# Performance work log

Hardware: AMD Instinct MI355X
Metric: run time of the kernel (lower is better)

The kernel has to match this reference:

```python
import jax, jax.numpy as jnp
import numpy as np

N_HEAD = 16


def setup_inputs() -> dict:
    key = jax.random.key(0)
    k1, k2, k3 = jax.random.split(key, 3)
    B, T, C = 4, 1024, 1024
    x = jax.random.normal(k1, (B, T, C), dtype=jnp.float32)
    w_attn = jax.random.normal(k2, (3 * C, C), dtype=jnp.float32) * 0.02
    w_proj = jax.random.normal(k3, (C, C), dtype=jnp.float32) * 0.02
    return {"x": x, "w_attn": w_attn, "w_proj": w_proj}


def reference(x, w_attn, w_proj):
    B, T, C = x.shape
    H = N_HEAD
    hs = C // H
    scale = 1.0 / np.sqrt(hs).astype(np.float32)

    qkv = x @ w_attn.T                         # [B, T, 3C]
    q, k, v = jnp.split(qkv, 3, axis=-1)
    q = q.reshape(B, T, H, hs).transpose(0, 2, 1, 3)   # [B, H, T, hs]
    k = k.reshape(B, T, H, hs).transpose(0, 2, 1, 3)
    v = v.reshape(B, T, H, hs).transpose(0, 2, 1, 3)

    scores = jnp.einsum('bhqd,bhkd->bhqk', q, k) * scale   # [B, H, T, T]
    causal = jnp.tril(jnp.ones((T, T), dtype=bool))
    scores = jnp.where(causal, scores, -jnp.inf)

    att = jax.nn.sigmoid(scores)                # sigmoid attention, not softmax
    # Bernoulli straight-through sampling (value = sample, grad flows via att)
    samp_key = jax.random.fold_in(jax.random.key(0), 42)
    samples = jax.random.bernoulli(samp_key, att).astype(att.dtype)
    att = att + jax.lax.stop_gradient(samples - att)

    y = jnp.einsum('bhqk,bhkd->bhqd', att, v)   # [B, H, T, hs]
    att_sum = att.sum(axis=-1)                  # [B, H, T]
    att_var = (att * (1.0 - att)).sum(axis=-1)  # [B, H, T]

    y = y.transpose(0, 2, 1, 3).reshape(B, T, C)
    y = y @ w_proj.T
    return (y, att_sum, att_var)
```

## Files before the change

kernel.cpp:

```cpp
#include <hip/hip_runtime.h>
#include <stdint.h>


#define T_SEQ 1024
#define QKV_LD 3072

typedef __attribute__((ext_vector_type(8))) short bf16x8;
typedef __attribute__((ext_vector_type(4))) float f32x4;
typedef __attribute__((ext_vector_type(4))) unsigned int u32x4;

typedef __attribute__((address_space(3))) uint32_t lds_u32;
typedef __attribute__((address_space(1))) const uint32_t g_u32;

#define ROTL(x, d) __builtin_amdgcn_alignbit((x), (x), 32 - (d))

__device__ __forceinline__ void threefry2x32(uint32_t k0, uint32_t k1,
                                             uint32_t x0, uint32_t x1,
                                             uint32_t &o0, uint32_t &o1) {
  uint32_t ks2 = k0 ^ k1 ^ 0x1BD11BDAu;
#define TF_R4(a, b, c, d)                                                      \
  x0 += x1; x1 = ROTL(x1, a); x1 ^= x0;                                        \
  x0 += x1; x1 = ROTL(x1, b); x1 ^= x0;                                        \
  x0 += x1; x1 = ROTL(x1, c); x1 ^= x0;                                        \
  x0 += x1; x1 = ROTL(x1, d); x1 ^= x0;
  x0 += k0; x1 += k1;
  TF_R4(13, 15, 26, 6)
  x0 += k1; x1 += ks2 + 1u;
  TF_R4(17, 29, 16, 24)
  x0 += ks2; x1 += k0 + 2u;
  TF_R4(13, 15, 26, 6)
  x0 += k0; x1 += k1 + 3u;
  TF_R4(17, 29, 16, 24)
  x0 += k1; x1 += ks2 + 4u;
  TF_R4(13, 15, 26, 6)
  x0 += ks2; x1 += k0 + 5u;
  o0 = x0; o1 = x1;
#undef TF_R4
}

__device__ __forceinline__ unsigned short f2bf(float f) {
  uint32_t u = __float_as_uint(f);
  u += 0x7FFFu + ((u >> 16) & 1u);
  return (unsigned short)(u >> 16);
}

#define N_X4  1048576
#define N_WA4 786432
#define N_WP4 262144

__global__ __launch_bounds__(256) void cvt3_bf16(const float4* __restrict__ x,
                                                 const float4* __restrict__ wa,
                                                 const float4* __restrict__ wp,
                                                 uint2* __restrict__ out) {
  size_t i = (size_t)blockIdx.x * 256 + threadIdx.x;
  const float4* src;
  size_t off;
  if (i < N_X4) { src = x; off = i; }
  else if (i < N_X4 + N_WA4) { src = wa; off = i - N_X4; }
  else { src = wp; off = i - (N_X4 + N_WA4); }
  float4 v = src[off];
  uint2 o;
  o.x = (uint32_t)f2bf(v.x) | ((uint32_t)f2bf(v.y) << 16);
  o.y = (uint32_t)f2bf(v.z) | ((uint32_t)f2bf(v.w) << 16);
  out[i] = o;
}

template <int OUT_BF16>
__global__ __launch_bounds__(256) void gemm_bf16(const unsigned short* __restrict__ A,
                                                 const unsigned short* __restrict__ B,
                                                 void* __restrict__ Cout,
                                                 int M, int N, int K) {
  __shared__ unsigned short As[128 * 32];
  __shared__ unsigned short Bs[128 * 32];

  const int t = threadIdx.x;
  const int lane = t & 63, w = t >> 6;
  const int g = lane >> 4, lr = lane & 15;
  const int rw = w >> 1, cw = w & 1;
  const int bm = blockIdx.x * 128, bn = blockIdx.y * 128;

  const unsigned short* Ag = A + (size_t)(bm + 32 * w + (lane >> 2)) * K + 8 * (lane & 3);
  const unsigned short* Bg = B + (size_t)(bn + 32 * w + (lane >> 2)) * K + 8 * (lane & 3);
  lds_u32* Al0 = (lds_u32*)&As[(32 * w) * 32];
  lds_u32* Al1 = (lds_u32*)&As[(32 * w + 16) * 32];
  lds_u32* Bl0 = (lds_u32*)&Bs[(32 * w) * 32];
  lds_u32* Bl1 = (lds_u32*)&Bs[(32 * w + 16) * 32];

  f32x4 acc[4][4];
#pragma unroll
  for (int i = 0; i < 4; ++i)
#pragma unroll
    for (int j = 0; j < 4; ++j) acc[i][j] = (f32x4){0.f, 0.f, 0.f, 0.f};

  for (int k0 = 0; k0 < K; k0 += 32) {
    __syncthreads();
    __builtin_amdgcn_global_load_lds((g_u32*)(const void*)(Ag + k0), Al0, 16, 0, 0);
    __builtin_amdgcn_global_load_lds((g_u32*)(const void*)(Ag + k0 + (size_t)16 * K), Al1, 16, 0, 0);
    __builtin_amdgcn_global_load_lds((g_u32*)(const void*)(Bg + k0), Bl0, 16, 0, 0);
    __builtin_amdgcn_global_load_lds((g_u32*)(const void*)(Bg + k0 + (size_t)16 * K), Bl1, 16, 0, 0);
    __syncthreads();

    bf16x8 af[4], bfr[4];
#pragma unroll
    for (int i = 0; i < 4; ++i)
      af[i] = *(const bf16x8*)&As[(64 * rw + 16 * i + lr) * 32 + 8 * g];
#pragma unroll
    for (int j = 0; j < 4; ++j)
      bfr[j] = *(const bf16x8*)&Bs[(64 * cw + 16 * j + lr) * 32 + 8 * g];
#pragma unroll
    for (int i = 0; i < 4; ++i)
#pragma unroll
      for (int j = 0; j < 4; ++j)
        acc[i][j] = __builtin_amdgcn_mfma_f32_16x16x32_bf16(af[i], bfr[j], acc[i][j], 0, 0, 0);
  }

#pragma unroll
  for (int i = 0; i < 4; ++i)
#pragma unroll
    for (int j = 0; j < 4; ++j)
#pragma unroll
      for (int r = 0; r < 4; ++r) {
        const size_t row = bm + 64 * rw + 16 * i + 4 * g + r;
        const size_t col = bn + 64 * cw + 16 * j + lr;
        if (OUT_BF16)
          ((unsigned short*)Cout)[row * N + col] = f2bf(acc[i][j][r]);
        else
          ((float*)Cout)[row * N + col] = acc[i][j][r];
      }
}

__constant__ uint8_t QT_OF[136] = {
    0, 1, 1, 2, 2, 2, 3, 3, 3, 3, 4, 4, 4, 4, 4, 5, 5, 5, 5, 5, 5,
    6, 6, 6, 6, 6, 6, 6, 7, 7, 7, 7, 7, 7, 7, 7,
    8, 8, 8, 8, 8, 8, 8, 8, 8, 9, 9, 9, 9, 9, 9, 9, 9, 9, 9,
    10, 10, 10, 10, 10, 10, 10, 10, 10, 10, 10,
    11, 11, 11, 11, 11, 11, 11, 11, 11, 11, 11, 11,
    12, 12, 12, 12, 12, 12, 12, 12, 12, 12, 12, 12, 12,
    13, 13, 13, 13, 13, 13, 13, 13, 13, 13, 13, 13, 13, 13,
    14, 14, 14, 14, 14, 14, 14, 14, 14, 14, 14, 14, 14, 14, 14,
    15, 15, 15, 15, 15, 15, 15, 15, 15, 15, 15, 15, 15, 15, 15, 15};

#define TFI_STEP(a)                                                            \
  _Pragma("unroll")                                                            \
  for (int j = 0; j < 4; ++j) {                                                \
    X0[j] += X1[j]; X1[j] = ROTL(X1[j], a); X1[j] ^= X0[j];                    \
  }
#define TFI_R4(a, b, c, d) TFI_STEP(a) TFI_STEP(b) TFI_STEP(c) TFI_STEP(d)
#define TFI_INJ(i0, i1)                                                        \
  _Pragma("unroll")                                                            \
  for (int j = 0; j < 4; ++j) { X0[j] += (i0); X1[j] += (i1); }

__global__ __launch_bounds__(256, 8) void attn_sample(const unsigned short* __restrict__ qkv,
                                                      unsigned short* __restrict__ Pbits) {
  __shared__ uint32_t Ks4[64 * 32];

  const int t = threadIdx.x;
  const int lane = t & 63, w = t >> 6;
  const int g = lane >> 4, lr = lane & 15;
  const int bid = blockIdx.x;
  const int bh = 8 * (bid & 7) + ((bid >> 3) & 7);
  const int id = bid >> 6;
  const int qt = QT_OF[id];
  const int kt = id - ((qt * (qt + 1)) >> 1);
  const int b = bh >> 4, h = bh & 15;
  const int q0 = qt * 64 + 16 * w;
  const int kt64 = kt * 64;
  const bool diag = (kt == qt);

  uint32_t dk0, dk1;
  threefry2x32(0u, 0u, 0u, 42u, dk0, dk1);
  const uint32_t ks2 = dk0 ^ dk1 ^ 0x1BD11BDAu;

  const unsigned short* kb = qkv + (size_t)(b * T_SEQ + kt64) * QKV_LD + 1024 + h * 64;
  {
    const int r = t >> 2, s4 = t & 3;
    const unsigned short* src = kb + (size_t)r * QKV_LD + 8 * s4;
    u32x4 v0 = *(const u32x4*)(src);
    u32x4 v1 = *(const u32x4*)(src + 32);
    const int sw = (r & 7) << 2;
    *(u32x4*)&Ks4[r * 32 + ((4 * s4) ^ sw)] = v0;
    *(u32x4*)&Ks4[r * 32 + ((4 * s4 + 16) ^ sw)] = v1;
  }
  const unsigned short* qr = qkv + (size_t)(b * T_SEQ + q0 + lr) * QKV_LD + h * 64 + 8 * g;
  const bf16x8 aq0 = *(const bf16x8*)qr;
  const bf16x8 aq1 = *(const bf16x8*)(qr + 32);
  __syncthreads();

  const int swzr = (lr & 7) << 2;
  unsigned short* prow = Pbits + ((size_t)((bh << 10) + q0)) * 64 + kt * 4;

#pragma unroll
  for (int c = 0; c < 4; ++c) {
    bool pred[4] = {false, false, false, false};
    if (!diag || c <= w) {
      const uint32_t* krow = &Ks4[(16 * c + lr) * 32];
      bf16x8 bk0 = *(const bf16x8*)&krow[(4 * g) ^ swzr];
      bf16x8 bk1 = *(const bf16x8*)&krow[(4 * g + 16) ^ swzr];
      f32x4 sa = __builtin_amdgcn_mfma_f32_16x16x32_bf16(aq0, bk0, (f32x4){0.f, 0.f, 0.f, 0.f}, 0, 0, 0);
      sa = __builtin_amdgcn_mfma_f32_16x16x32_bf16(aq1, bk1, sa, 0, 0, 0);

      const int kg = kt64 + 16 * c + lr;
      const uint32_t idxc =
          ((uint32_t)bh << 20) | ((uint32_t)(q0 + 4 * g) << 10) | (uint32_t)kg;

      float e[4];
#pragma unroll
      for (int r = 0; r < 4; ++r)
        e[r] = __builtin_exp2f(sa[r] * -0.18033688011112042f);

      uint32_t X0[4], X1[4];
#pragma unroll
      for (int r = 0; r < 4; ++r) { X0[r] = dk0; X1[r] = idxc + ((uint32_t)r << 10) + dk1; }
      TFI_R4(13, 15, 26, 6)
      TFI_INJ(dk1, ks2 + 1u)
      TFI_R4(17, 29, 16, 24)
      TFI_INJ(ks2, dk0 + 2u)
      TFI_R4(13, 15, 26, 6)
      TFI_INJ(dk0, dk1 + 3u)
      TFI_R4(17, 29, 16, 24)
      TFI_INJ(dk1, ks2 + 4u)
      TFI_R4(13, 15, 26, 6)
      TFI_INJ(ks2, dk0 + 5u)

#pragma unroll
      for (int r = 0; r < 4; ++r) {
        const int qg = q0 + 4 * g + r;
        float u = __uint_as_float(0x3F800000u | ((X0[r] ^ X1[r]) >> 9)) - 1.0f;
        pred[r] = (fmaf(u, e[r], u) < 1.0f) & (kg <= qg);
      }
    }
#pragma unroll
    for (int r = 0; r < 4; ++r) {
      unsigned long long m = __ballot(pred[r]);
      if (lr == 0)
        prow[(size_t)(4 * g + r) * 64 + c] = (unsigned short)((m >> (16 * g)) & 0xFFFFu);
    }
  }
}

__global__ __launch_bounds__(256) void attn_pv(const unsigned short* __restrict__ qkv,
                                               const unsigned short* __restrict__ Pbits,
                                               unsigned short* __restrict__ yatt,
                                               float* __restrict__ att_sum,
                                               float* __restrict__ att_var) {
  __shared__ uint32_t Vt4[64 * 32];

  const int t = threadIdx.x;
  const int lane = t & 63, w = t >> 6;
  const int g = lane >> 4, lr = lane & 15;
  const int bid = blockIdx.x;
  const int bh = 8 * (bid & 7) + ((bid >> 3) & 7);
  const int qt = 15 - (bid >> 6);
  const int b = bh >> 4, h = bh & 15;
  const int q0 = qt * 64 + 16 * w;

  const int swzr = (lr & 7) << 2;
  const unsigned short* prow = Pbits + ((size_t)((bh << 10) + q0 + lr)) * 64;

  f32x4 yacc[4];
#pragma unroll
  for (int c = 0; c < 4; ++c) yacc[c] = (f32x4){0.f, 0.f, 0.f, 0.f};
  uint32_t rs = 0;

#pragma unroll 1
  for (int kt = 0; kt <= qt; ++kt) {
    __syncthreads();
    {
      const int k2 = 2 * (t & 31), d0 = 8 * (t >> 5);
      const unsigned short* vsrc =
          qkv + (size_t)(b * T_SEQ + kt * 64 + k2) * QKV_LD + 2048 + h * 64 + d0;
      union { u32x4 v; unsigned short us[8]; } va, vb2;
      va.v = *(const u32x4*)(vsrc);
      vb2.v = *(const u32x4*)(vsrc + QKV_LD);
#pragma unroll
      for (int jj = 0; jj < 8; ++jj) {
        uint32_t pw = (uint32_t)va.us[jj] | ((uint32_t)vb2.us[jj] << 16);
        Vt4[(d0 + jj) * 32 + ((t & 31) ^ ((jj & 7) << 2))] = pw;
      }
    }
    __syncthreads();

    const uint64_t bits = *(const uint64_t*)(prow + kt * 4);
    rs += (uint32_t)__popcll(bits);

#pragma unroll
    for (int ks = 0; ks < 2; ++ks) {
      const uint32_t byte = (uint32_t)(bits >> (32 * ks + 8 * g)) & 0xFFu;
      union { uint32_t u[4]; bf16x8 v; } pa;
#pragma unroll
      for (int j = 0; j < 4; ++j) {
        pa.u[j] = ((byte >> (2 * j)) & 1u ? 0x3F80u : 0u) |
                  ((byte >> (2 * j + 1)) & 1u ? 0x3F800000u : 0u);
      }
#pragma unroll
      for (int c = 0; c < 4; ++c) {
        bf16x8 vb = *(const bf16x8*)&Vt4[(16 * c + lr) * 32 + ((4 * g + 16 * ks) ^ swzr)];
        yacc[c] = __builtin_amdgcn_mfma_f32_16x16x32_bf16(pa.v, vb, yacc[c], 0, 0, 0);
      }
    }
  }

  const size_t yb = (size_t)(b * T_SEQ + q0) * 1024 + h * 64;
#pragma unroll
  for (int c = 0; c < 4; ++c)
#pragma unroll
    for (int r = 0; r < 4; ++r)
      yatt[yb + (size_t)(4 * g + r) * 1024 + 16 * c + lr] = f2bf(yacc[c][r]);

  if (g == 0) att_sum[(size_t)bh * T_SEQ + q0 + lr] = (float)rs;
  if (lane < 16) att_var[(size_t)bh * T_SEQ + q0 + lane] = 0.f;
}

extern "C" void kernel_launch(void* const* d_in, const int* in_sizes, int n_in,
                              void* d_out, int out_size, void* d_ws, size_t ws_size,
                              hipStream_t stream) {
  (void)in_sizes; (void)n_in; (void)out_size; (void)ws_size;
  const float* x      = (const float*)d_in[0];
  const float* w_attn = (const float*)d_in[1];
  const float* w_proj = (const float*)d_in[2];

  float* y_out      = (float*)d_out;
  float* attsum_out = y_out + (size_t)4 * 1024 * 1024;
  float* attvar_out = attsum_out + (size_t)4 * 16 * 1024;

  unsigned short* ws_us = (unsigned short*)d_ws;
  unsigned short* x_bf    = ws_us;
  unsigned short* wa_bf   = x_bf + (size_t)4 * 1024 * 1024;
  unsigned short* wp_bf   = wa_bf + (size_t)3 * 1024 * 1024;
  unsigned short* qkv_bf  = wp_bf + (size_t)1024 * 1024;
  unsigned short* yatt_bf = qkv_bf + (size_t)4096 * 3072;
  unsigned short* pbits   = yatt_bf + (size_t)4096 * 1024;

  dim3 blk(256);
  cvt3_bf16<<<dim3(8192), blk, 0, stream>>>((const float4*)x, (const float4*)w_attn,
                                            (const float4*)w_proj, (uint2*)x_bf);
  gemm_bf16<1><<<dim3(32, 24), blk, 0, stream>>>(x_bf, wa_bf, (void*)qkv_bf, 4096, 3072, 1024);
  attn_sample<<<dim3(8704), blk, 0, stream>>>(qkv_bf, pbits);
  attn_pv<<<dim3(1024), blk, 0, stream>>>(qkv_bf, pbits, yatt_bf, attsum_out, attvar_out);
  gemm_bf16<0><<<dim3(32, 8), blk, 0, stream>>>(yatt_bf, wp_bf, (void*)y_out, 4096, 1024, 1024);
}
```

Measured before the change: 173.1 us.

## Pair causal query tiles per block in PV and simplify diagonal masking in sampling

The PV kernel now runs 512 blocks, and each block handles two query tiles (qt = 15-p and qt = p), so every block does the same total number of key tiles. This balances the triangular causal workload across blocks. In the sampling kernel, the causal mask for diagonal tiles is applied as a precomputed bitmask on the ballot result instead of a per-lane comparison, and the branch uses a wave-uniform index. Skipped chunks write zero directly. The risk is that halving the grid lowers occupancy and adds a serial second pass per block.

```diff
diff --git a/kernel.cpp b/kernel.cpp
--- a/kernel.cpp
+++ b/kernel.cpp
@@ -140,16 +140,6 @@
     14, 14, 14, 14, 14, 14, 14, 14, 14, 14, 14, 14, 14, 14, 14,
     15, 15, 15, 15, 15, 15, 15, 15, 15, 15, 15, 15, 15, 15, 15, 15};
 
-#define TFI_STEP(a)                                                            \
-  _Pragma("unroll")                                                            \
-  for (int j = 0; j < 4; ++j) {                                                \
-    X0[j] += X1[j]; X1[j] = ROTL(X1[j], a); X1[j] ^= X0[j];                    \
-  }
-#define TFI_R4(a, b, c, d) TFI_STEP(a) TFI_STEP(b) TFI_STEP(c) TFI_STEP(d)
-#define TFI_INJ(i0, i1)                                                        \
-  _Pragma("unroll")                                                            \
-  for (int j = 0; j < 4; ++j) { X0[j] += (i0); X1[j] += (i1); }
-
 __global__ __launch_bounds__(256, 8) void attn_sample(const unsigned short* __restrict__ qkv,
                                                       unsigned short* __restrict__ Pbits) {
   __shared__ uint32_t Ks4[64 * 32];
@@ -166,6 +156,7 @@
   const int q0 = qt * 64 + 16 * w;
   const int kt64 = kt * 64;
   const bool diag = (kt == qt);
+  const int ws = __builtin_amdgcn_readfirstlane(w);
 
   uint32_t dk0, dk1;
   threefry2x32(0u, 0u, 0u, 42u, dk0, dk1);
@@ -189,10 +180,19 @@
   const int swzr = (lr & 7) << 2;
   unsigned short* prow = Pbits + ((size_t)((bh << 10) + q0)) * 64 + kt * 4;
 
+#define TFI_STEP(a)                                                            \
+  _Pragma("unroll")                                                            \
+  for (int j = 0; j < 4; ++j) {                                                \
+    X0[j] += X1[j]; X1[j] = ROTL(X1[j], a); X1[j] ^= X0[j];                    \
+  }
+#define TFI_R4(a, b, c, d) TFI_STEP(a) TFI_STEP(b) TFI_STEP(c) TFI_STEP(d)
+#define TFI_INJ(i0, i1)                                                        \
+  _Pragma("unroll")                                                            \
+  for (int j = 0; j < 4; ++j) { X0[j] += (i0); X1[j] += (i1); }
+
 #pragma unroll
   for (int c = 0; c < 4; ++c) {
-    bool pred[4] = {false, false, false, false};
-    if (!diag || c <= w) {
+    if (!diag || c <= ws) {
       const uint32_t* krow = &Ks4[(16 * c + lr) * 32];
       bf16x8 bk0 = *(const bf16x8*)&krow[(4 * g) ^ swzr];
       bf16x8 bk1 = *(const bf16x8*)&krow[(4 * g + 16) ^ swzr];
@@ -224,18 +224,31 @@
 
 #pragma unroll
       for (int r = 0; r < 4; ++r) {
-        const int qg = q0 + 4 * g + r;
         float u = __uint_as_float(0x3F800000u | ((X0[r] ^ X1[r]) >> 9)) - 1.0f;
-        pred[r] = (fmaf(u, e[r], u) < 1.0f) & (kg <= qg);
+        unsigned long long m = __ballot(fmaf(u, e[r], u) < 1.0f);
+        if (diag) {
+          const int d = 16 * (ws - c) + r;
+          unsigned long long cm = 0ull;
+#pragma unroll
+          for (int gg = 0; gg < 4; ++gg) {
+            const int thr = d + 4 * gg;
+            const uint32_t pc = (thr >= 15) ? 0xFFFFu : ((2u << thr) - 1u);
+            cm |= (unsigned long long)pc << (16 * gg);
+          }
+          m &= cm;
+        }
+        if (lr == 0)
+          prow[(size_t)(4 * g + r) * 64 + c] = (unsigned short)(m >> (16 * g));
       }
+    } else {
+#pragma unroll
+      for (int r = 0; r < 4; ++r)
+        if (lr == 0) prow[(size_t)(4 * g + r) * 64 + c] = 0;
     }
-#pragma unroll
-    for (int r = 0; r < 4; ++r) {
-      unsigned long long m = __ballot(pred[r]);
-      if (lr == 0)
-        prow[(size_t)(4 * g + r) * 64 + c] = (unsigned short)((m >> (16 * g)) & 0xFFFFu);
-    }
-  }
+  }
+#undef TFI_STEP
+#undef TFI_R4
+#undef TFI_INJ
 }
 
 __global__ __launch_bounds__(256) void attn_pv(const unsigned short* __restrict__ qkv,
@@ -250,65 +263,69 @@
   const int g = lane >> 4, lr = lane & 15;
   const int bid = blockIdx.x;
   const int bh = 8 * (bid & 7) + ((bid >> 3) & 7);
-  const int qt = 15 - (bid >> 6);
+  const int p = bid >> 6;
   const int b = bh >> 4, h = bh & 15;
-  const int q0 = qt * 64 + 16 * w;
-
   const int swzr = (lr & 7) << 2;
-  const unsigned short* prow = Pbits + ((size_t)((bh << 10) + q0 + lr)) * 64;
-
-  f32x4 yacc[4];
-#pragma unroll
-  for (int c = 0; c < 4; ++c) yacc[c] = (f32x4){0.f, 0.f, 0.f, 0.f};
-  uint32_t rs = 0;
 
 #pragma unroll 1
-  for (int kt = 0; kt <= qt; ++kt) {
-    __syncthreads();
-    {
-      const int k2 = 2 * (t & 31), d0 = 8 * (t >> 5);
-      const unsigned short* vsrc =
-          qkv + (size_t)(b * T_SEQ + kt * 64 + k2) * QKV_LD + 2048 + h * 64 + d0;
-      union { u32x4 v; unsigned short us[8]; } va, vb2;
-      va.v = *(const u32x4*)(vsrc);
-      vb2.v = *(const u32x4*)(vsrc + QKV_LD);
-#pragma unroll
-      for (int jj = 0; jj < 8; ++jj) {
-        uint32_t pw = (uint32_t)va.us[jj] | ((uint32_t)vb2.us[jj] << 16);
-        Vt4[(d0 + jj) * 32 + ((t & 31) ^ ((jj & 7) << 2))] = pw;
+  for (int half = 0; half < 2; ++half) {
+    const int qt = half ? p : 15 - p;
+    const int q0 = qt * 64 + 16 * w;
+    const unsigned short* prow = Pbits + ((size_t)((bh << 10) + q0 + lr)) * 64;
+
+    f32x4 yacc[4];
+#pragma unroll
+    for (int c = 0; c < 4; ++c) yacc[c] = (f32x4){0.f, 0.f, 0.f, 0.f};
+    uint32_t rs = 0;
+
+#pragma unroll 1
+    for (int kt = 0; kt <= qt; ++kt) {
+      __syncthreads();
+      {
+        const int k2 = 2 * (t & 31), d0 = 8 * (t >> 5);
+        const unsigned short* vsrc =
+            qkv + (size_t)(b * T_SEQ + kt * 64 + k2) * QKV_LD + 2048 + h * 64 + d0;
+        union { u32x4 v; unsigned short us[8]; } va, vb2;
+        va.v = *(const u32x4*)(vsrc);
+        vb2.v = *(const u32x4*)(vsrc + QKV_LD);
+#pragma unroll
+        for (int jj = 0; jj < 8; ++jj) {
+          uint32_t pw = (uint32_t)va.us[jj] | ((uint32_t)vb2.us[jj] << 16);
+          Vt4[(d0 + jj) * 32 + ((t & 31) ^ ((jj & 7) << 2))] = pw;
+        }
+      }
+      __syncthreads();
+
+      const uint64_t bits = *(const uint64_t*)(prow + kt * 4);
+      rs += (uint32_t)__popcll(bits);
+
+#pragma unroll
+      for (int ks = 0; ks < 2; ++ks) {
+        const uint32_t byte = (uint32_t)(bits >> (32 * ks + 8 * g)) & 0xFFu;
+        union { uint32_t u[4]; bf16x8 v; } pa;
+#pragma unroll
+        for (int j = 0; j < 4; ++j) {
+          pa.u[j] = ((byte >> (2 * j)) & 1u ? 0x3F80u : 0u) |
+                    ((byte >> (2 * j + 1)) & 1u ? 0x3F800000u : 0u);
+        }
+#pragma unroll
+        for (int c = 0; c < 4; ++c) {
+          bf16x8 vb = *(const bf16x8*)&Vt4[(16 * c + lr) * 32 + ((4 * g + 16 * ks) ^ swzr)];
+          yacc[c] = __builtin_amdgcn_mfma_f32_16x16x32_bf16(pa.v, vb, yacc[c], 0, 0, 0);
+        }
       }
     }
-    __syncthreads();
-
-    const uint64_t bits = *(const uint64_t*)(prow + kt * 4);
-    rs += (uint32_t)__popcll(bits);
-
-#pragma unroll
-    for (int ks = 0; ks < 2; ++ks) {
-      const uint32_t byte = (uint32_t)(bits >> (32 * ks + 8 * g)) & 0xFFu;
-      union { uint32_t u[4]; bf16x8 v; } pa;
-#pragma unroll
-      for (int j = 0; j < 4; ++j) {
-        pa.u[j] = ((byte >> (2 * j)) & 1u ? 0x3F80u : 0u) |
-                  ((byte >> (2 * j + 1)) & 1u ? 0x3F800000u : 0u);
-      }
-#pragma unroll
-      for (int c = 0; c < 4; ++c) {
-        bf16x8 vb = *(const bf16x8*)&Vt4[(16 * c + lr) * 32 + ((4 * g + 16 * ks) ^ swzr)];
-        yacc[c] = __builtin_amdgcn_mfma_f32_16x16x32_bf16(pa.v, vb, yacc[c], 0, 0, 0);
-      }
-    }
-  }
-
-  const size_t yb = (size_t)(b * T_SEQ + q0) * 1024 + h * 64;
-#pragma unroll
-  for (int c = 0; c < 4; ++c)
-#pragma unroll
-    for (int r = 0; r < 4; ++r)
-      yatt[yb + (size_t)(4 * g + r) * 1024 + 16 * c + lr] = f2bf(yacc[c][r]);
-
-  if (g == 0) att_sum[(size_t)bh * T_SEQ + q0 + lr] = (float)rs;
-  if (lane < 16) att_var[(size_t)bh * T_SEQ + q0 + lane] = 0.f;
+
+    const size_t yb = (size_t)(b * T_SEQ + q0) * 1024 + h * 64;
+#pragma unroll
+    for (int c = 0; c < 4; ++c)
+#pragma unroll
+      for (int r = 0; r < 4; ++r)
+        yatt[yb + (size_t)(4 * g + r) * 1024 + 16 * c + lr] = f2bf(yacc[c][r]);
+
+    if (g == 0) att_sum[(size_t)bh * T_SEQ + q0 + lr] = (float)rs;
+    if (lane < 16) att_var[(size_t)bh * T_SEQ + q0 + lane] = 0.f;
+  }
 }
 
 extern "C" void kernel_launch(void* const* d_in, const int* in_sizes, int n_in,
@@ -336,6 +353,6 @@
                                             (const float4*)w_proj, (uint2*)x_bf);
   gemm_bf16<1><<<dim3(32, 24), blk, 0, stream>>>(x_bf, wa_bf, (void*)qkv_bf, 4096, 3072, 1024);
   attn_sample<<<dim3(8704), blk, 0, stream>>>(qkv_bf, pbits);
-  attn_pv<<<dim3(1024), blk, 0, stream>>>(qkv_bf, pbits, yatt_bf, attsum_out, attvar_out);
+  attn_pv<<<dim3(512), blk, 0, stream>>>(qkv_bf, pbits, yatt_bf, attsum_out, attvar_out);
   gemm_bf16<0><<<dim3(32, 8), blk, 0, stream>>>(yatt_bf, wp_bf, (void*)y_out, 4096, 1024, 1024);
 }
```

Result: no change. 169.7 us (-2.0%).
